# Performance work log

Hardware: AMD Instinct MI355X
Metric: run time of the kernel (lower is better)

## Reference

```python
import jax, jax.numpy as jnp
import numpy as np

B, S, D, H = 2, 2048, 1024, 16
DK = D // H


def setup_inputs() -> dict:
    key = jax.random.key(0)
    ks = jax.random.split(key, 8)
    query = jax.random.normal(ks[0], (B, S, D), dtype=jnp.float32)
    key_t = jax.random.normal(ks[1], (B, S, D), dtype=jnp.float32)
    value = jax.random.normal(ks[2], (B, S, D), dtype=jnp.float32)
    # causal mask (1 = attend, 0 = masked), broadcast over batch and heads
    mask = jnp.tril(jnp.ones((S, S), dtype=jnp.int32))[None, None, :, :]
    scale = 1.0 / np.sqrt(D)
    w_q = jax.random.normal(ks[3], (D, D), dtype=jnp.float32) * scale
    w_k = jax.random.normal(ks[4], (D, D), dtype=jnp.float32) * scale
    w_v = jax.random.normal(ks[5], (D, D), dtype=jnp.float32) * scale
    w_o = jax.random.normal(ks[6], (D, D), dtype=jnp.float32) * scale
    b_o = jnp.zeros((D,), dtype=jnp.float32)
    return {"query": query, "key": key_t, "value": value, "mask": mask,
            "w_q": w_q, "w_k": w_k, "w_v": w_v, "w_o": w_o, "b_o": b_o}


def reference(query, key, value, mask, w_q, w_k, w_v, w_o, b_o):
    # projections: nn.Linear applies x @ W.T; weights here stored as [out, in]
    def proj(x, w):  # [B,S,D] -> [B,H,S,DK]
        y = jnp.einsum('bsd,ed->bse', x, w)
        return y.reshape(B, S, H, DK).transpose(0, 2, 1, 3)

    Q = proj(query, w_q)
    K = proj(key, w_k)
    V = proj(value, w_v)

    scores = jnp.einsum('bhqd,bhkd->bhqk', Q, K) / jnp.sqrt(jnp.float32(DK))
    scores = jnp.where(mask == 0, jnp.float32(-1e9), scores)
    attention_weights = jax.nn.softmax(scores, axis=-1)  # dropout p=0 (eval)
    context = jnp.einsum('bhqk,bhkd->bhqd', attention_weights, V)
    context = context.transpose(0, 2, 1, 3).reshape(B, S, D)
    output = jnp.einsum('bsd,ed->bse', context, w_o) + b_o
    return output, attention_weights
```

## Files before the change

### kernel.cpp

```cpp
#include <hip/hip_runtime.h>
#include <hip/hip_bf16.h>
#include <math.h>

#define B_  2
#define S_  2048
#define D_  1024
#define H_  16
#define DK_ 64

typedef __attribute__((ext_vector_type(8))) short bf16x8;
typedef __attribute__((ext_vector_type(4))) float f32x4;
typedef __attribute__((ext_vector_type(8))) unsigned short u16x8;
typedef __attribute__((ext_vector_type(4))) unsigned short u16x4;

#define MFMA16(a, b, c) __builtin_amdgcn_mfma_f32_16x16x32_bf16((a), (b), (c), 0, 0, 0)

__device__ __forceinline__ unsigned short f2bf(float f) {
    union { float f; unsigned u; } v; v.f = f;
    unsigned r = v.u + 0x7fffu + ((v.u >> 16) & 1u);
    return (unsigned short)(r >> 16);
}
__device__ __forceinline__ float bf2f(unsigned short u) {
    return __uint_as_float(((unsigned)u) << 16);
}

__global__ __launch_bounds__(256) void cvt_all(
        const float* __restrict__ q, const float* __restrict__ k, const float* __restrict__ v,
        const float* __restrict__ wq, const float* __restrict__ wk,
        const float* __restrict__ wv, const float* __restrict__ wo,
        unsigned short* __restrict__ xq, unsigned short* __restrict__ xk,
        unsigned short* __restrict__ xv, unsigned short* __restrict__ wqb,
        unsigned short* __restrict__ wkb, unsigned short* __restrict__ wvb,
        unsigned short* __restrict__ wob) {
    int i = blockIdx.x * 256 + threadIdx.x;
    const float* src; unsigned short* dst; int off;
    if      (i < 1048576) { src = q;  dst = xq;  off = 0; }
    else if (i < 2097152) { src = k;  dst = xk;  off = 1048576; }
    else if (i < 3145728) { src = v;  dst = xv;  off = 2097152; }
    else if (i < 3407872) { src = wq; dst = wqb; off = 3145728; }
    else if (i < 3670016) { src = wk; dst = wkb; off = 3407872; }
    else if (i < 3932160) { src = wv; dst = wvb; off = 3670016; }
    else                  { src = wo; dst = wob; off = 3932160; }
    i -= off;
    f32x4 f = __builtin_nontemporal_load(reinterpret_cast<const f32x4*>(src) + i);
    ushort4 o;
    o.x = f2bf(f[0]); o.y = f2bf(f[1]); o.z = f2bf(f[2]); o.w = f2bf(f[3]);
    reinterpret_cast<ushort4*>(dst)[i] = o;
}

__device__ __forceinline__ void gemm_bt_body(char* myep, int blk,
        const unsigned short* __restrict__ A, const unsigned short* __restrict__ W,
        void* __restrict__ out, const float* __restrict__ bias, int mode, float scale) {
    const int lane = threadIdx.x & 63;
    const int row  = lane & 15, quad = lane >> 4;
    const int w    = threadIdx.x >> 6;
    const int bmi  = blk & 31;
    const int bni  = blk >> 5;
    const int m0   = bmi * 128 + (w >> 1) * 64;
    const int n0   = bni * 128 + (w & 1) * 64;
    f32x4 acc[4][4] = {};
    const unsigned short* Ap = A + (m0 + row) * D_ + quad * 8;
    const unsigned short* Wp = W + (n0 + row) * D_ + quad * 8;
    for (int k0 = 0; k0 < D_; k0 += 32) {
        bf16x8 a0 = *(const bf16x8*)(Ap + k0);
        bf16x8 a1 = *(const bf16x8*)(Ap + 16 * D_ + k0);
        bf16x8 a2 = *(const bf16x8*)(Ap + 32 * D_ + k0);
        bf16x8 a3 = *(const bf16x8*)(Ap + 48 * D_ + k0);
        bf16x8 w0 = *(const bf16x8*)(Wp + k0);
        bf16x8 w1 = *(const bf16x8*)(Wp + 16 * D_ + k0);
        bf16x8 w2 = *(const bf16x8*)(Wp + 32 * D_ + k0);
        bf16x8 w3 = *(const bf16x8*)(Wp + 48 * D_ + k0);
        acc[0][0] = MFMA16(a0, w0, acc[0][0]);
        acc[0][1] = MFMA16(a0, w1, acc[0][1]);
        acc[0][2] = MFMA16(a0, w2, acc[0][2]);
        acc[0][3] = MFMA16(a0, w3, acc[0][3]);
        acc[1][0] = MFMA16(a1, w0, acc[1][0]);
        acc[1][1] = MFMA16(a1, w1, acc[1][1]);
        acc[1][2] = MFMA16(a1, w2, acc[1][2]);
        acc[1][3] = MFMA16(a1, w3, acc[1][3]);
        acc[2][0] = MFMA16(a2, w0, acc[2][0]);
        acc[2][1] = MFMA16(a2, w1, acc[2][1]);
        acc[2][2] = MFMA16(a2, w2, acc[2][2]);
        acc[2][3] = MFMA16(a2, w3, acc[2][3]);
        acc[3][0] = MFMA16(a3, w0, acc[3][0]);
        acc[3][1] = MFMA16(a3, w1, acc[3][1]);
        acc[3][2] = MFMA16(a3, w2, acc[3][2]);
        acc[3][3] = MFMA16(a3, w3, acc[3][3]);
    }
    const int b = m0 >> 11;
    const int h = n0 >> 6;
    if (mode == 0) {
        unsigned short* lt = (unsigned short*)myep;
#pragma unroll
        for (int mi = 0; mi < 4; mi++)
#pragma unroll
            for (int t = 0; t < 4; t++)
#pragma unroll
                for (int r = 0; r < 4; r++)
                    lt[(mi * 16 + quad * 4 + r) * 72 + t * 16 + row] = f2bf(acc[mi][t][r] * scale);
        __builtin_amdgcn_sched_barrier(0);
        unsigned short* Qout = (unsigned short*)out;
#pragma unroll
        for (int pass = 0; pass < 8; pass++) {
            int rr = pass * 8 + (lane >> 3);
            int cc = (lane & 7) * 8;
            u16x8 val = *(const u16x8*)(lt + rr * 72 + cc);
            int s = (m0 + rr) & (S_ - 1);
            *(u16x8*)(&Qout[(((size_t)(b * H_ + h)) * S_ + s) * DK_ + cc]) = val;
        }
    } else if (mode == 1) {
        unsigned short* lt = (unsigned short*)myep;
#pragma unroll
        for (int mi = 0; mi < 4; mi++)
#pragma unroll
            for (int t = 0; t < 4; t++)
#pragma unroll
                for (int r = 0; r < 4; r++)
                    lt[(t * 16 + row) * 72 + mi * 16 + quad * 4 + r] = f2bf(acc[mi][t][r]);
        __builtin_amdgcn_sched_barrier(0);
        unsigned short* Vout = (unsigned short*)out;
#pragma unroll
        for (int pass = 0; pass < 8; pass++) {
            int dk = pass * 8 + (lane >> 3);
            int so = (lane & 7) * 8;
            u16x8 val = *(const u16x8*)(lt + dk * 72 + so);
            *(u16x8*)(&Vout[(((size_t)(b * H_ + h)) * DK_ + dk) * S_ + (m0 & (S_ - 1)) + so]) = val;
        }
    } else {
        float* lt32 = (float*)myep;
        float bs[4];
#pragma unroll
        for (int t = 0; t < 4; t++) bs[t] = bias[n0 + t * 16 + row];
        float* outF = (float*)out;
#pragma unroll
        for (int mh = 0; mh < 2; mh++) {
#pragma unroll
            for (int mi2 = 0; mi2 < 2; mi2++)
#pragma unroll
                for (int t = 0; t < 4; t++)
#pragma unroll
                    for (int r = 0; r < 4; r++)
                        lt32[(mi2 * 16 + quad * 4 + r) * 72 + t * 16 + row] =
                            acc[mh * 2 + mi2][t][r] + bs[t];
            __builtin_amdgcn_sched_barrier(0);
#pragma unroll
            for (int pass = 0; pass < 8; pass++) {
                int rr = pass * 4 + (lane >> 4);
                int cc = (lane & 15) * 4;
                f32x4 val = *(const f32x4*)(lt32 + rr * 72 + cc);
                __builtin_nontemporal_store(val,
                    (f32x4*)(&outF[(size_t)(m0 + mh * 32 + rr) * D_ + n0 + cc]));
            }
            __builtin_amdgcn_sched_barrier(0);
        }
    }
}

__global__ __launch_bounds__(256) void gemm_qkv(
        const unsigned short* __restrict__ xq, const unsigned short* __restrict__ xk,
        const unsigned short* __restrict__ xv, const unsigned short* __restrict__ wqb,
        const unsigned short* __restrict__ wkb, const unsigned short* __restrict__ wvb,
        unsigned short* __restrict__ Qb, unsigned short* __restrict__ Kb,
        unsigned short* __restrict__ Vt) {
    __shared__ char eplds[4 * 9216];
    char* myep = eplds + (threadIdx.x >> 6) * 9216;
    const int which = blockIdx.x >> 8;
    const int blk   = blockIdx.x & 255;
    if (which == 0)      gemm_bt_body(myep, blk, xq, wqb, Qb, nullptr, 0, 0.125f);
    else if (which == 1) gemm_bt_body(myep, blk, xk, wkb, Kb, nullptr, 0, 1.0f);
    else                 gemm_bt_body(myep, blk, xv, wvb, Vt, nullptr, 1, 1.0f);
}

__global__ __launch_bounds__(256) void gemm_out(
        const unsigned short* __restrict__ A, const unsigned short* __restrict__ W,
        float* __restrict__ out, const float* __restrict__ bias) {
    __shared__ char eplds[4 * 9216];
    gemm_bt_body(eplds + (threadIdx.x >> 6) * 9216, blockIdx.x, A, W, out, bias, 2, 1.0f);
}

__global__ __launch_bounds__(256) void attn_kernel(const unsigned short* __restrict__ Qb,
                                                   const unsigned short* __restrict__ Kb,
                                                   const unsigned short* __restrict__ Vt,
                                                   float* __restrict__ Pbase,
                                                   unsigned short* __restrict__ ctx) {
    __shared__ unsigned short plds[4][16 * 40];
    __shared__ float olds[4][16 * 64];
    __shared__ float llds[4][16];
    const int w    = threadIdx.x >> 6;
    const int lane = threadIdx.x & 63;
    const int row  = lane & 15, quad = lane >> 4;
    const int tile = 127 - (int)(blockIdx.x >> 5);
    const int bh   = blockIdx.x & 31;
    const int q0   = tile * 16;
    const int b    = bh >> 4, h = bh & 15;
    const unsigned short* Qh = Qb + (size_t)bh * S_ * DK_;
    const unsigned short* Kh = Kb + (size_t)bh * S_ * DK_;
    const unsigned short* Vh = Vt + (size_t)bh * DK_ * S_;
    float* P = Pbase + (size_t)bh * S_ * S_;

    bf16x8 aq0 = *(const bf16x8*)(Qh + (q0 + row) * DK_ + quad * 8);
    bf16x8 aq1 = *(const bf16x8*)(Qh + (q0 + row) * DK_ + 32 + quad * 8);

    const int nks   = (q0 + 47) >> 5;
    const int nfull = (q0 + 1) >> 5;

    float l_l[4] = {0.f, 0.f, 0.f, 0.f};
    for (int ks = w; ks < nks; ks += 4) {
        const int c0k = ks * 32;
        const bool diag = (ks >= nfull);
#pragma unroll
        for (int half = 0; half < 2; half++) {
            const int c = c0k + half * 16;
            const unsigned short* kp = Kh + (c + row) * DK_ + quad * 8;
            bf16x8 k0 = *(const bf16x8*)kp;
            bf16x8 k1 = *(const bf16x8*)(kp + 32);
            f32x4 sa = {};
            sa = MFMA16(aq0, k0, sa);
            sa = MFMA16(aq1, k1, sa);
#pragma unroll
            for (int r = 0; r < 4; r++) {
                float p = __expf(sa[r]);
                if (diag) p = ((c + row) <= (q0 + quad * 4 + r)) ? p : 0.f;
                l_l[r] += p;
            }
        }
    }
#pragma unroll
    for (int r = 0; r < 4; r++) {
#pragma unroll
        for (int off = 1; off < 16; off <<= 1)
            l_l[r] += __shfl_xor(l_l[r], off, 16);
        if (row == 0) llds[w][quad * 4 + r] = l_l[r];
    }
    __syncthreads();
    float invL[4];
#pragma unroll
    for (int r = 0; r < 4; r++)
        invL[r] = 1.0f / (llds[0][quad * 4 + r] + llds[1][quad * 4 + r] +
                          llds[2][quad * 4 + r] + llds[3][quad * 4 + r]);

    f32x4 o[4] = {};
    unsigned short* myld = plds[w];
    for (int ks = w; ks < nks; ks += 4) {
        const int c0k = ks * 32;
        const bool diag = (ks >= nfull);
#pragma unroll
        for (int half = 0; half < 2; half++) {
            const int c = c0k + half * 16;
            const unsigned short* kp = Kh + (c + row) * DK_ + quad * 8;
            bf16x8 k0 = *(const bf16x8*)kp;
            bf16x8 k1 = *(const bf16x8*)(kp + 32);
            f32x4 sa = {};
            sa = MFMA16(aq0, k0, sa);
            sa = MFMA16(aq1, k1, sa);
#pragma unroll
            for (int r = 0; r < 4; r++) {
                float p = __expf(sa[r]) * invL[r];
                if (diag) p = ((c + row) <= (q0 + quad * 4 + r)) ? p : 0.f;
                myld[(quad * 4 + r) * 40 + half * 16 + row] = f2bf(p);
            }
        }
        __builtin_amdgcn_sched_barrier(0);
#pragma unroll
        for (int g = 0; g < 2; g++) {
            int rr = g * 8 + (lane >> 3);
            int cg = (lane & 7) * 4;
            u16x4 pb = *(const u16x4*)(myld + rr * 40 + cg);
            f32x4 pv;
            pv[0] = bf2f((unsigned short)pb[0]);
            pv[1] = bf2f((unsigned short)pb[1]);
            pv[2] = bf2f((unsigned short)pb[2]);
            pv[3] = bf2f((unsigned short)pb[3]);
            __builtin_nontemporal_store(pv, (f32x4*)(&P[(size_t)(q0 + rr) * S_ + c0k + cg]));
        }
        bf16x8 pf = *(const bf16x8*)(myld + row * 40 + quad * 8);
#pragma unroll
        for (int t4 = 0; t4 < 4; t4++) {
            bf16x8 vv = *(const bf16x8*)(Vh + (t4 * 16 + row) * S_ + c0k + quad * 8);
            o[t4] = MFMA16(pf, vv, o[t4]);
        }
        __builtin_amdgcn_sched_barrier(0);
    }

    float* myo = olds[w];
#pragma unroll
    for (int t4 = 0; t4 < 4; t4++)
#pragma unroll
        for (int r = 0; r < 4; r++)
            myo[(quad * 4 + r) * 64 + t4 * 16 + row] = o[t4][r];
    __syncthreads();
    {
        int i  = threadIdx.x;
        int rr = i >> 4, c4 = (i & 15) * 4;
        u16x4 cv;
#pragma unroll
        for (int j = 0; j < 4; j++) {
            float s = olds[0][rr * 64 + c4 + j] + olds[1][rr * 64 + c4 + j] +
                      olds[2][rr * 64 + c4 + j] + olds[3][rr * 64 + c4 + j];
            cv[j] = (short)f2bf(s);
        }
        *(u16x4*)(&ctx[((size_t)(b * S_) + q0 + rr) * D_ + h * DK_ + c4]) = cv;
    }

    const int cb = nks * 32;
    if (cb < S_) {
        const f32x4 z = {0.f, 0.f, 0.f, 0.f};
#pragma unroll 1
        for (int rr = 0; rr < 16; rr++) {
            float* Pr = &P[(size_t)(q0 + rr) * S_];
            for (int cc = cb + threadIdx.x * 4; cc < S_; cc += 1024)
                __builtin_nontemporal_store(z, reinterpret_cast<f32x4*>(Pr + cc));
        }
    }
}

extern "C" void kernel_launch(void* const* d_in, const int* in_sizes, int n_in,
                              void* d_out, int out_size, void* d_ws, size_t ws_size,
                              hipStream_t stream) {
    const float* q  = (const float*)d_in[0];
    const float* k  = (const float*)d_in[1];
    const float* v  = (const float*)d_in[2];
    const float* wq = (const float*)d_in[4];
    const float* wk = (const float*)d_in[5];
    const float* wv = (const float*)d_in[6];
    const float* wo = (const float*)d_in[7];
    const float* bo = (const float*)d_in[8];

    unsigned short* ws  = (unsigned short*)d_ws;
    unsigned short* xq  = ws;
    unsigned short* xk  = ws + 4194304;
    unsigned short* xv  = ws + 8388608;
    unsigned short* wqb = ws + 12582912;
    unsigned short* wkb = wqb + 1048576;
    unsigned short* wvb = wkb + 1048576;
    unsigned short* wob = wvb + 1048576;
    unsigned short* Qb  = ws + 16777216;
    unsigned short* Kb  = Qb + 4194304;
    unsigned short* Vt  = Kb + 4194304;
    unsigned short* ctx = Vt + 4194304;
    float* outp  = (float*)d_out;
    float* Pbase = outp + 4194304;

    cvt_all<<<16384, 256, 0, stream>>>(q, k, v, wq, wk, wv, wo,
                                       xq, xk, xv, wqb, wkb, wvb, wob);

    gemm_qkv<<<768, 256, 0, stream>>>(xq, xk, xv, wqb, wkb, wvb, Qb, Kb, Vt);

    attn_kernel<<<4096, 256, 0, stream>>>(Qb, Kb, Vt, Pbase, ctx);

    gemm_out<<<256, 256, 0, stream>>>(ctx, wob, outp, bo);
}
```

Baseline: 858.4 us.

## Stage GEMM A/W tiles through LDS with direct global-to-LDS loads

The projection GEMM body now cooperatively loads each 128x32 slice of A and W into shared memory using global_load_lds, and each wave then reads its MFMA fragments from LDS. Before, each wave loaded its operands straight from global memory. This removes the duplicate global loads across waves that share rows and columns. The cost is two block-wide barriers per k-step with no double buffering, so load latency is not overlapped with MFMA work. The epilogue reuses the same shared buffer after the loop.

```diff
diff --git a/kernel.cpp b/kernel.cpp
--- a/kernel.cpp
+++ b/kernel.cpp
@@ -22,6 +22,12 @@
 }
 __device__ __forceinline__ float bf2f(unsigned short u) {
     return __uint_as_float(((unsigned)u) << 16);
+}
+
+__device__ __forceinline__ void gload16(const unsigned short* g, unsigned short* l) {
+    __builtin_amdgcn_global_load_lds(
+        (const __attribute__((address_space(1))) unsigned int*)g,
+        (__attribute__((address_space(3))) unsigned int*)l, 16, 0, 0);
 }
 
 __global__ __launch_bounds__(256) void cvt_all(
@@ -48,7 +54,7 @@
     reinterpret_cast<ushort4*>(dst)[i] = o;
 }
 
-__device__ __forceinline__ void gemm_bt_body(char* myep, int blk,
+__device__ __forceinline__ void gemm_bt_body(char* smem, int blk,
         const unsigned short* __restrict__ A, const unsigned short* __restrict__ W,
         void* __restrict__ out, const float* __restrict__ bias, int mode, float scale) {
     const int lane = threadIdx.x & 63;
@@ -56,20 +62,42 @@
     const int w    = threadIdx.x >> 6;
     const int bmi  = blk & 31;
     const int bni  = blk >> 5;
-    const int m0   = bmi * 128 + (w >> 1) * 64;
-    const int n0   = bni * 128 + (w & 1) * 64;
+    const int m0b  = bmi * 128, n0b = bni * 128;
+    const int m0   = m0b + (w >> 1) * 64;
+    const int n0   = n0b + (w & 1) * 64;
+
+    unsigned short* Ab = (unsigned short*)smem;
+    unsigned short* Wb = Ab + 4096;
+
+    const int c0    = w * 2;
+    const int srow  = c0 * 16 + (lane >> 2);
+    const int scol  = (lane & 3) * 8;
+    const unsigned short* gA0 = A + (size_t)(m0b + srow) * D_ + scol;
+    const unsigned short* gA1 = gA0 + 16 * D_;
+    const unsigned short* gW0 = W + (size_t)(n0b + srow) * D_ + scol;
+    const unsigned short* gW1 = gW0 + 16 * D_;
+    unsigned short* lA0 = Ab + c0 * 512;
+    unsigned short* lA1 = lA0 + 512;
+    unsigned short* lW0 = Wb + c0 * 512;
+    unsigned short* lW1 = lW0 + 512;
+
+    const int arow = (w >> 1) * 64 + row;
+    const int wrow = (w & 1) * 64 + row;
     f32x4 acc[4][4] = {};
-    const unsigned short* Ap = A + (m0 + row) * D_ + quad * 8;
-    const unsigned short* Wp = W + (n0 + row) * D_ + quad * 8;
     for (int k0 = 0; k0 < D_; k0 += 32) {
-        bf16x8 a0 = *(const bf16x8*)(Ap + k0);
-        bf16x8 a1 = *(const bf16x8*)(Ap + 16 * D_ + k0);
-        bf16x8 a2 = *(const bf16x8*)(Ap + 32 * D_ + k0);
-        bf16x8 a3 = *(const bf16x8*)(Ap + 48 * D_ + k0);
-        bf16x8 w0 = *(const bf16x8*)(Wp + k0);
-        bf16x8 w1 = *(const bf16x8*)(Wp + 16 * D_ + k0);
-        bf16x8 w2 = *(const bf16x8*)(Wp + 32 * D_ + k0);
-        bf16x8 w3 = *(const bf16x8*)(Wp + 48 * D_ + k0);
+        gload16(gA0 + k0, lA0);
+        gload16(gA1 + k0, lA1);
+        gload16(gW0 + k0, lW0);
+        gload16(gW1 + k0, lW1);
+        __syncthreads();
+        bf16x8 a0 = *(const bf16x8*)(Ab + (arow     ) * 32 + quad * 8);
+        bf16x8 a1 = *(const bf16x8*)(Ab + (arow + 16) * 32 + quad * 8);
+        bf16x8 a2 = *(const bf16x8*)(Ab + (arow + 32) * 32 + quad * 8);
+        bf16x8 a3 = *(const bf16x8*)(Ab + (arow + 48) * 32 + quad * 8);
+        bf16x8 w0 = *(const bf16x8*)(Wb + (wrow     ) * 32 + quad * 8);
+        bf16x8 w1 = *(const bf16x8*)(Wb + (wrow + 16) * 32 + quad * 8);
+        bf16x8 w2 = *(const bf16x8*)(Wb + (wrow + 32) * 32 + quad * 8);
+        bf16x8 w3 = *(const bf16x8*)(Wb + (wrow + 48) * 32 + quad * 8);
         acc[0][0] = MFMA16(a0, w0, acc[0][0]);
         acc[0][1] = MFMA16(a0, w1, acc[0][1]);
         acc[0][2] = MFMA16(a0, w2, acc[0][2]);
@@ -86,7 +114,10 @@
         acc[3][1] = MFMA16(a3, w1, acc[3][1]);
         acc[3][2] = MFMA16(a3, w2, acc[3][2]);
         acc[3][3] = MFMA16(a3, w3, acc[3][3]);
-    }
+        __syncthreads();
+    }
+
+    char* myep = smem + w * 9216;
     const int b = m0 >> 11;
     const int h = n0 >> 6;
     if (mode == 0) {
@@ -162,20 +193,19 @@
         const unsigned short* __restrict__ wkb, const unsigned short* __restrict__ wvb,
         unsigned short* __restrict__ Qb, unsigned short* __restrict__ Kb,
         unsigned short* __restrict__ Vt) {
-    __shared__ char eplds[4 * 9216];
-    char* myep = eplds + (threadIdx.x >> 6) * 9216;
+    __shared__ char smem[36864];
     const int which = blockIdx.x >> 8;
     const int blk   = blockIdx.x & 255;
-    if (which == 0)      gemm_bt_body(myep, blk, xq, wqb, Qb, nullptr, 0, 0.125f);
-    else if (which == 1) gemm_bt_body(myep, blk, xk, wkb, Kb, nullptr, 0, 1.0f);
-    else                 gemm_bt_body(myep, blk, xv, wvb, Vt, nullptr, 1, 1.0f);
+    if (which == 0)      gemm_bt_body(smem, blk, xq, wqb, Qb, nullptr, 0, 0.125f);
+    else if (which == 1) gemm_bt_body(smem, blk, xk, wkb, Kb, nullptr, 0, 1.0f);
+    else                 gemm_bt_body(smem, blk, xv, wvb, Vt, nullptr, 1, 1.0f);
 }
 
 __global__ __launch_bounds__(256) void gemm_out(
         const unsigned short* __restrict__ A, const unsigned short* __restrict__ W,
         float* __restrict__ out, const float* __restrict__ bias) {
-    __shared__ char eplds[4 * 9216];
-    gemm_bt_body(eplds + (threadIdx.x >> 6) * 9216, blockIdx.x, A, W, out, bias, 2, 1.0f);
+    __shared__ char smem[36864];
+    gemm_bt_body(smem, blockIdx.x, A, W, out, bias, 2, 1.0f);
 }
 
 __global__ __launch_bounds__(256) void attn_kernel(const unsigned short* __restrict__ Qb,
```

Measured after the change: 765.3 us. 1.12x faster.
